# Kernel tuning notes

Hardware: AMD Instinct MI355X
Metric: run time of the kernel (lower is better)

The kernel has to match this reference:

```python
import jax, jax.numpy as jnp
import numpy as np

B, S, D = 2, 2048, 1024
H = 16
HD = D // H  # 64

def setup_inputs() -> dict:
    key = jax.random.key(0)
    ks = jax.random.split(key, 6)
    scale = 0.02
    x   = jax.random.normal(ks[0], (B, S, D), dtype=jnp.float32)
    Wq  = jax.random.normal(ks[1], (D, D), dtype=jnp.float32) * scale
    Wk  = jax.random.normal(ks[2], (D, D), dtype=jnp.float32) * scale
    Wv  = jax.random.normal(ks[3], (D, D), dtype=jnp.float32) * scale
    Wo  = jax.random.normal(ks[4], (D, D), dtype=jnp.float32) * scale
    bo  = jax.random.normal(ks[5], (D,), dtype=jnp.float32) * scale
    return {"x": x, "Wq": Wq, "Wk": Wk, "Wv": Wv, "Wo": Wo, "bo": bo}

def reference(x, Wq, Wk, Wv, Wo, bo):
    b, s, d = x.shape
    # QKV projections (no bias, qkv_bias=False); weights stored as [d_in, d_out]
    q = (x @ Wq).reshape(b, s, H, HD).transpose(0, 2, 1, 3)  # [b,h,s,hd]
    k = (x @ Wk).reshape(b, s, H, HD).transpose(0, 2, 1, 3)
    v = (x @ Wv).reshape(b, s, H, HD).transpose(0, 2, 1, 3)
    scores = jnp.einsum('bhqd,bhkd->bhqk', q, k)  # [b,h,s,s]
    causal = jnp.triu(jnp.ones((s, s), dtype=bool), k=1)
    scores = jnp.where(causal, -jnp.inf, scores)
    attn = jax.nn.softmax(scores / jnp.sqrt(jnp.float32(HD)), axis=-1)
    # dropout_rate = 0.0 -> identity
    ctx = jnp.einsum('bhqk,bhkd->bqhd', attn, v).reshape(b, s, d)
    return ctx @ Wo + bo
```

## Files before the change

### kernel.cpp

```cpp
#include <hip/hip_runtime.h>
#include <hip/hip_bf16.h>
#include <math.h>

#define B_ 2
#define S_ 2048
#define D_ 1024
#define H_ 16
#define HD_ 64
#define M_ (B_*S_)

typedef __attribute__((ext_vector_type(8))) short bf16x8;
typedef __attribute__((ext_vector_type(4))) float f32x4;
typedef __attribute__((ext_vector_type(16))) float f32x16;

#define MFMA16(a,b,c) __builtin_amdgcn_mfma_f32_16x16x32_bf16(a,b,c,0,0,0)
#define MFMA32(a,b,c) __builtin_amdgcn_mfma_f32_32x32x16_bf16(a,b,c,0,0,0)
#define INFF __builtin_inff()
#define LOG2E 1.44269504088896340736f
#define EXP2F(x) __builtin_amdgcn_exp2f(x)

static __device__ __forceinline__ unsigned short f2bf_bits(float f) {
    unsigned int u = __float_as_uint(f);
    unsigned int r = (u + 0x7fffu + ((u >> 16) & 1u)) >> 16;
    return (unsigned short)r;
}

static __device__ __forceinline__ unsigned cvt_pk_bf16(float a, float b) {
    unsigned r;
    asm("v_cvt_pk_bf16_f32 %0, %1, %2" : "=v"(r) : "v"(a), "v"(b));
    return r;
}

static __device__ __forceinline__ void gload16(const unsigned short* g, unsigned short* l) {
    __builtin_amdgcn_global_load_lds(
        (const __attribute__((address_space(1))) unsigned int*)(g),
        (__attribute__((address_space(3))) unsigned int*)(l),
        16, 0, 0);
}

#define BARR do { \
    __builtin_amdgcn_sched_barrier(0); \
    __builtin_amdgcn_s_barrier(); \
    __builtin_amdgcn_sched_barrier(0); \
} while (0)
#define LGK0 do { \
    asm volatile("s_waitcnt lgkmcnt(0)" ::: "memory"); \
    __builtin_amdgcn_sched_barrier(0); \
} while (0)
#define LGK8 do { \
    asm volatile("s_waitcnt lgkmcnt(8)" ::: "memory"); \
    __builtin_amdgcn_sched_barrier(0); \
} while (0)
#define VM6 do { \
    asm volatile("s_waitcnt vmcnt(6)" ::: "memory"); \
    __builtin_amdgcn_sched_barrier(0); \
} while (0)

__global__ __launch_bounds__(256) void convert_x_kernel(
    const float* __restrict__ x, unsigned short* __restrict__ o) {
    size_t i = (size_t)blockIdx.x * 256 + threadIdx.x;
    float4 v = reinterpret_cast<const float4*>(x)[i];
    ushort4 u;
    u.x = f2bf_bits(v.x); u.y = f2bf_bits(v.y);
    u.z = f2bf_bits(v.z); u.w = f2bf_bits(v.w);
    reinterpret_cast<ushort4*>(o)[i] = u;
}

__global__ __launch_bounds__(256) void convw_kernel(
    const float* __restrict__ W0, const float* __restrict__ W1,
    const float* __restrict__ W2, const float* __restrict__ W3,
    unsigned short* __restrict__ OT) {
    __shared__ float t[32][33];
    const float* W = (blockIdx.z == 0) ? W0 : (blockIdx.z == 1) ? W1
                    : (blockIdx.z == 2) ? W2 : W3;
    unsigned short* O = OT + (size_t)blockIdx.z * D_ * D_;
    int tx = threadIdx.x & 31, ty = threadIdx.x >> 5;
    int kb = blockIdx.y * 32, nb = blockIdx.x * 32;
#pragma unroll
    for (int i = 0; i < 4; i++)
        t[ty + 8*i][tx] = W[(size_t)(kb + ty + 8*i) * D_ + nb + tx];
    __syncthreads();
#pragma unroll
    for (int i = 0; i < 4; i++) {
        int n = nb + ty + 8*i, k = kb + tx;
        O[(size_t)n * D_ + k] = f2bf_bits(t[tx][ty + 8*i]);
    }
}

__global__ __launch_bounds__(512, 2) void gemm_qkv256(
    const unsigned short* __restrict__ A,
    const unsigned short* __restrict__ BT,
    unsigned short* __restrict__ outp)
{
    __shared__ union {
        struct { unsigned short A[2][2][8192]; unsigned short B[2][2][8192]; } s;
        unsigned short vt[256][136];
    } sm;
    const int tid = threadIdx.x, lane = tid & 63, wid = tid >> 6;
    const int lrow = lane & 15, lk8 = lane >> 4, orow = lk8 * 4;
    const int wmo = (wid >> 2) * 64;
    const int wno = (wid & 3) * 32;
    const int m0 = blockIdx.x * 256, n0 = blockIdx.y * 256;

    const int srow = lane >> 3, sgr = lane & 7;
    const unsigned sgo = (unsigned)(wid * 8 + srow) * 1024u
                       + (unsigned)((sgr ^ srow) << 3);
    const unsigned short* Ag = A  + (unsigned)m0 * 1024u + sgo;
    const unsigned short* Bg = BT + (unsigned)n0 * 1024u + sgo;
    const int ldsrb = wid * 512;

    const int sw0 = ((lk8 ^ (lrow & 7)) << 3);
    const int sw1 = (((4 | lk8) ^ (lrow & 7)) << 3);
    int ar[4], br[2];
#pragma unroll
    for (int f = 0; f < 4; f++) ar[f] = (wmo + f * 16 + lrow) * 64;
#pragma unroll
    for (int g = 0; g < 2; g++) br[g] = (wno + g * 16 + lrow) * 64;

    f32x4 acc[8][4] = {};
    bf16x8 af[4][2], bf0[2][2], bf1[2][2];

    auto stA = [&](int par, int mh, unsigned k) {
        unsigned short* d = &sm.s.A[par][mh][ldsrb];
        const unsigned short* g = Ag + (unsigned)mh * 131072u + k;
        gload16(g, d);
        gload16(g + 65536u, d + 4096);
    };
    auto stB = [&](int par, int nh, unsigned k) {
        unsigned short* d = &sm.s.B[par][nh][ldsrb];
        const unsigned short* g = Bg + (unsigned)nh * 131072u + k;
        gload16(g, d);
        gload16(g + 65536u, d + 4096);
    };
    auto lda = [&](int par, int mh) {
        const unsigned short* p = &sm.s.A[par][mh][0];
#pragma unroll
        for (int f = 0; f < 4; f++) {
            af[f][0] = *reinterpret_cast<const bf16x8*>(p + ar[f] + sw0);
            af[f][1] = *reinterpret_cast<const bf16x8*>(p + ar[f] + sw1);
        }
    };
    auto ldb0 = [&](int par, int nh) {
        const unsigned short* p = &sm.s.B[par][nh][0];
#pragma unroll
        for (int g = 0; g < 2; g++) {
            bf0[g][0] = *reinterpret_cast<const bf16x8*>(p + br[g] + sw0);
            bf0[g][1] = *reinterpret_cast<const bf16x8*>(p + br[g] + sw1);
        }
    };
    auto ldb1 = [&](int par, int nh) {
        const unsigned short* p = &sm.s.B[par][nh][0];
#pragma unroll
        for (int g = 0; g < 2; g++) {
            bf1[g][0] = *reinterpret_cast<const bf16x8*>(p + br[g] + sw0);
            bf1[g][1] = *reinterpret_cast<const bf16x8*>(p + br[g] + sw1);
        }
    };
    auto MMA0 = [&](int mh) {
        __builtin_amdgcn_s_setprio(1);
#pragma unroll
        for (int f = 0; f < 4; f++)
#pragma unroll
            for (int g = 0; g < 2; g++)
#pragma unroll
                for (int ks = 0; ks < 2; ks++)
                    acc[mh*4+f][g] = MFMA16(af[f][ks], bf0[g][ks], acc[mh*4+f][g]);
        __builtin_amdgcn_s_setprio(0);
    };
    auto MMA1 = [&](int mh) {
        __builtin_amdgcn_s_setprio(1);
#pragma unroll
        for (int f = 0; f < 4; f++)
#pragma unroll
            for (int g = 0; g < 2; g++)
#pragma unroll
                for (int ks = 0; ks < 2; ks++)
                    acc[mh*4+f][2+g] = MFMA16(af[f][ks], bf1[g][ks], acc[mh*4+f][2+g]);
        __builtin_amdgcn_s_setprio(0);
    };

    stA(0, 0, 0);  stB(0, 0, 0);  stB(0, 1, 0);  stA(0, 1, 0);
    stA(1, 0, 64); stB(1, 0, 64); stB(1, 1, 64);
    VM6; BARR;

#pragma unroll 1
    for (int i = 0; i < 8; i++) {
        const unsigned kA1 = (unsigned)(2*i + 1) * 64u;
        const unsigned k2  = (unsigned)((2*i + 2) & 15) * 64u;
        const unsigned k3  = (unsigned)((2*i + 3) & 15) * 64u;
        lda(0, 0); ldb0(0, 0); stA(1, 1, kA1);
        LGK8; BARR; LGK0; MMA0(0); BARR;
        ldb1(0, 1); stA(0, 0, k2);
        BARR; LGK0; MMA1(0); BARR;
        lda(0, 1); stB(0, 0, k2);
        BARR; LGK0; MMA1(1); BARR;
        stB(0, 1, k2);
        VM6; BARR; MMA0(1); BARR;
        lda(1, 0); ldb0(1, 0); stA(0, 1, k2);
        LGK8; BARR; LGK0; MMA0(0); BARR;
        ldb1(1, 1); stA(1, 0, k3);
        BARR; LGK0; MMA1(0); BARR;
        lda(1, 1); stB(1, 0, k3);
        BARR; LGK0; MMA1(1); BARR;
        stB(1, 1, k3);
        VM6; BARR; MMA0(1); BARR;
    }

    asm volatile("s_waitcnt vmcnt(0)" ::: "memory");
    __builtin_amdgcn_sched_barrier(0);
    __builtin_amdgcn_s_barrier();

    const int which = n0 >> 10;
    const int nl0 = n0 & 1023;
    const int bq = m0 >> 11;
    unsigned short* obase = outp + (size_t)which * 4194304;

    if (which < 2) {
        const float scale = (which == 0) ? (0.125f * LOG2E) : 1.0f;
#pragma unroll
        for (int fi = 0; fi < 8; fi++)
#pragma unroll
            for (int g = 0; g < 4; g++)
#pragma unroll
                for (int r = 0; r < 4; r++) {
                    int m = m0 + (fi >> 2) * 128 + wmo + (fi & 3) * 16 + orow + r;
                    int n = nl0 + (g >> 1) * 128 + wno + (g & 1) * 16 + lrow;
                    int s = m & 2047;
                    obase[(((size_t)(bq * 16 + (n >> 6)) * 2048 + s) << 6) + (n & 63)]
                        = f2bf_bits(acc[fi][g][r] * scale);
                }
    } else {
#pragma unroll
        for (int qm = 0; qm < 2; qm++) {
#pragma unroll
            for (int f = 0; f < 4; f++)
#pragma unroll
                for (int g = 0; g < 4; g++) {
                    const int ml = wmo + f * 16 + orow;
                    const int nc = (g >> 1) * 128 + wno + (g & 1) * 16 + lrow;
                    uint2 w;
                    w.x = cvt_pk_bf16(acc[qm*4+f][g][0], acc[qm*4+f][g][1]);
                    w.y = cvt_pk_bf16(acc[qm*4+f][g][2], acc[qm*4+f][g][3]);
                    *reinterpret_cast<uint2*>(&sm.vt[nc][ml]) = w;
                }
            __syncthreads();
            {
                const int row = tid >> 1, c0 = (tid & 1) * 64;
                unsigned short* dst = obase +
                    ((size_t)(bq * 1024) + nl0 + row) * 2048 +
                    (m0 & 2047) + qm * 128 + c0;
#pragma unroll
                for (int j = 0; j < 64; j += 8)
                    *reinterpret_cast<bf16x8*>(dst + j) =
                        *reinterpret_cast<const bf16x8*>(&sm.vt[row][c0 + j]);
            }
            __syncthreads();
        }
    }
}

template<int BN, int MODE>
__global__ __launch_bounds__(256) void gemm_gl(
    const unsigned short* __restrict__ A,
    const unsigned short* __restrict__ BT,
    void* __restrict__ outp,
    const float* __restrict__ bias)
{
    constexpr int K = 1024;
    constexpr int NF = (BN == 128) ? 4 : 2;
    __shared__ struct { unsigned short As[128][64]; unsigned short Bs[BN][64]; } sm;
    const int m0 = blockIdx.x * 128;
    const int n0 = blockIdx.y * BN;
    const int tid = threadIdx.x, lane = tid & 63, wid = tid >> 6;
    const int wm = (wid >> 1) * 64;
    const int wn = (wid & 1) * (BN / 2);
    const int lrow = lane & 15, lk8 = lane >> 4, orow = lk8 * 4;
    f32x4 acc[4][NF] = {};

    for (int k0 = 0; k0 < K; k0 += 64) {
#pragma unroll
        for (int i = 0; i < 4; i++) {
            const int rbase = wid * 32 + i * 8;
            const int rl = rbase + (lane >> 3);
            const int sc = ((lane & 7) ^ (rl & 7)) << 3;
            gload16(A + (size_t)(m0 + rl) * K + k0 + sc, &sm.As[rbase][0]);
        }
#pragma unroll
        for (int i = 0; i < BN / 32; i++) {
            const int rbase = wid * (BN / 4) + i * 8;
            const int rl = rbase + (lane >> 3);
            const int sc = ((lane & 7) ^ (rl & 7)) << 3;
            gload16(BT + (size_t)(n0 + rl) * K + k0 + sc, &sm.Bs[rbase][0]);
        }
        __syncthreads();
#pragma unroll
        for (int ks = 0; ks < 2; ks++) {
            bf16x8 af[4], bfr[NF];
#pragma unroll
            for (int f = 0; f < 4; f++) {
                const int row = wm + f * 16 + lrow;
                const int p = (ks * 4 + lk8) ^ (row & 7);
                af[f] = *reinterpret_cast<const bf16x8*>(&sm.As[row][p * 8]);
            }
#pragma unroll
            for (int f = 0; f < NF; f++) {
                const int row = wn + f * 16 + lrow;
                const int p = (ks * 4 + lk8) ^ (row & 7);
                bfr[f] = *reinterpret_cast<const bf16x8*>(&sm.Bs[row][p * 8]);
            }
            __builtin_amdgcn_s_setprio(1);
#pragma unroll
            for (int mf = 0; mf < 4; mf++)
#pragma unroll
                for (int nf = 0; nf < NF; nf++)
                    acc[mf][nf] = MFMA16(af[mf], bfr[nf], acc[mf][nf]);
            __builtin_amdgcn_s_setprio(0);
        }
        __syncthreads();
    }

    float* o = (float*)outp;
#pragma unroll
    for (int mf = 0; mf < 4; mf++)
#pragma unroll
        for (int nf = 0; nf < NF; nf++)
#pragma unroll
            for (int r = 0; r < 4; r++) {
                int m = m0 + wm + mf*16 + orow + r;
                int n = n0 + wn + nf*16 + lrow;
                o[(size_t)m * 1024 + n] = acc[mf][nf][r] + bias[n];
            }
}

__global__ __launch_bounds__(256, 2) void attn_kernel(
    const unsigned short* __restrict__ Q,
    const unsigned short* __restrict__ Kb,
    const unsigned short* __restrict__ VT,
    unsigned short* __restrict__ ctx)
{
    __shared__ unsigned short Ks[2][64][64];
    __shared__ unsigned short Vs[2][64][64];
    const int fid = blockIdx.x;
    const int xcd = fid & 7, t = fid >> 3;
    const int bh = xcd | ((t & 3) << 3);
    const int qt = 15 - (t >> 2);
    const int lane = threadIdx.x & 63, wid = threadIdx.x >> 6;
    const int l31 = lane & 31, hi = lane >> 5;
    const unsigned short* Qp = Q  + (size_t)bh * (S_ * 64);
    const unsigned short* Kp = Kb + (size_t)bh * (S_ * 64);
    const unsigned short* Vp = VT + (size_t)bh * (64 * S_);
    const int b = bh >> 4, h = bh & 15;
    const int q0w = qt * 128 + wid * 32;
    const int qg  = q0w + l31;
    const int nb  = 2 * qt + 2;

    auto stage = [&](int buf, int kv0) {
#pragma unroll
        for (int i = 0; i < 2; i++) {
            const int rbase = wid * 16 + 8 * i;
            const int rl = rbase + (lane >> 3);
            const int sc = (((lane & 7) ^ (rl & 7)) << 3);
            gload16(Kp + (size_t)(kv0 + rl) * 64 + sc, &Ks[buf][rbase][0]);
            gload16(Vp + (size_t)rl * S_ + kv0 + sc, &Vs[buf][rbase][0]);
        }
    };

    stage(0, 0);

    bf16x8 qf[4];
#pragma unroll
    for (int c = 0; c < 4; c++)
        qf[c] = *reinterpret_cast<const bf16x8*>(
            Qp + (size_t)qg * 64 + c * 16 + hi * 8);

    f32x16 oacc0 = {}, oacc1 = {};
    float lr = 0.f;
    const int r0 = l31, r1 = 32 + l31;
    const int g0 = r0 & 7, g1 = r1 & 7;

    __syncthreads();

#pragma unroll 1
    for (int kvb = 0; kvb < nb; kvb++) {
        const int cur = kvb & 1;
        if (kvb + 1 < nb) stage(cur ^ 1, (kvb + 1) * 64);

        f32x16 s0 = {}, s1 = {};
        __builtin_amdgcn_s_setprio(1);
#pragma unroll
        for (int c = 0; c < 4; c++) {
            const int gg = (c << 1) | hi;
            bf16x8 k0 = *reinterpret_cast<const bf16x8*>(&Ks[cur][r0][(gg ^ g0) << 3]);
            bf16x8 k1 = *reinterpret_cast<const bf16x8*>(&Ks[cur][r1][(gg ^ g1) << 3]);
            s0 = MFMA32(k0, qf[c], s0);
            s1 = MFMA32(k1, qf[c], s1);
        }
        __builtin_amdgcn_s_setprio(0);

        if (kvb * 64 + 63 > q0w) {
            const int kvb64 = kvb * 64 + 4 * hi;
#pragma unroll
            for (int reg = 0; reg < 16; reg++) {
                const int kv = kvb64 + (reg & 3) + 8 * (reg >> 2);
                if (kv > qg)      s0[reg] = -INFF;
                if (kv + 32 > qg) s1[reg] = -INFF;
            }
        }

        float t0 = 0.f, t1 = 0.f;
#pragma unroll
        for (int reg = 0; reg < 16; reg++) {
            s0[reg] = EXP2F(s0[reg]);
            s1[reg] = EXP2F(s1[reg]);
            t0 += s0[reg];
            t1 += s1[reg];
        }
        lr += t0 + t1;

        bf16x8 pf[4];
#pragma unroll
        for (int c = 0; c < 4; c++) {
            const int rb = (c & 1) * 8;
            unsigned x0, x1, y0, y1;
            if (c < 2) {
                x0 = cvt_pk_bf16(s0[rb+0], s0[rb+1]);
                x1 = cvt_pk_bf16(s0[rb+2], s0[rb+3]);
                y0 = cvt_pk_bf16(s0[rb+4], s0[rb+5]);
                y1 = cvt_pk_bf16(s0[rb+6], s0[rb+7]);
            } else {
                x0 = cvt_pk_bf16(s1[rb+0], s1[rb+1]);
                x1 = cvt_pk_bf16(s1[rb+2], s1[rb+3]);
                y0 = cvt_pk_bf16(s1[rb+4], s1[rb+5]);
                y1 = cvt_pk_bf16(s1[rb+6], s1[rb+7]);
            }
            asm("v_permlane32_swap_b32 %0, %1" : "+v"(x0), "+v"(y0));
            asm("v_permlane32_swap_b32 %0, %1" : "+v"(x1), "+v"(y1));
            union { unsigned u[4]; bf16x8 v; } pk;
            pk.u[0] = x0; pk.u[1] = x1; pk.u[2] = y0; pk.u[3] = y1;
            pf[c] = pk.v;
        }

        __builtin_amdgcn_s_setprio(1);
#pragma unroll
        for (int c = 0; c < 4; c++) {
            const int gg = (c << 1) | hi;
            bf16x8 v0 = *reinterpret_cast<const bf16x8*>(&Vs[cur][r0][(gg ^ g0) << 3]);
            bf16x8 v1 = *reinterpret_cast<const bf16x8*>(&Vs[cur][r1][(gg ^ g1) << 3]);
            oacc0 = MFMA32(v0, pf[c], oacc0);
            oacc1 = MFMA32(v1, pf[c], oacc1);
        }
        __builtin_amdgcn_s_setprio(0);
        __syncthreads();
    }

    lr += __shfl_xor(lr, 32);
    const float inv = 1.0f / lr;
    unsigned short* crow = ctx + ((size_t)(b * S_ + qg)) * D_ + h * 64;
#pragma unroll
    for (int a = 0; a < 4; a++)
#pragma unroll
        for (int p = 0; p < 2; p++) {
            const int reg = 4 * a + 2 * p;
            const int col = 8 * a + 4 * hi + 2 * p;
            unsigned w0 = cvt_pk_bf16(oacc0[reg] * inv, oacc0[reg + 1] * inv);
            unsigned w1 = cvt_pk_bf16(oacc1[reg] * inv, oacc1[reg + 1] * inv);
            *reinterpret_cast<unsigned*>(crow + col)      = w0;
            *reinterpret_cast<unsigned*>(crow + 32 + col) = w1;
        }
}

extern "C" void kernel_launch(void* const* d_in, const int* in_sizes, int n_in,
                              void* d_out, int out_size, void* d_ws, size_t ws_size,
                              hipStream_t stream) {
    const float* x  = (const float*)d_in[0];
    const float* Wq = (const float*)d_in[1];
    const float* Wk = (const float*)d_in[2];
    const float* Wv = (const float*)d_in[3];
    const float* Wo = (const float*)d_in[4];
    const float* bo = (const float*)d_in[5];
    float* out = (float*)d_out;

    char* ws = (char*)d_ws;
    unsigned short* xb  = (unsigned short*)(ws);
    unsigned short* WT  = (unsigned short*)(ws + 8388608);
    unsigned short* QKV = (unsigned short*)(ws + 16777216);
    unsigned short* ctx = (unsigned short*)(ws + 41943040);

    unsigned short* Qb  = QKV;
    unsigned short* Kb  = QKV + 4194304;
    unsigned short* VTb = QKV + 8388608;

    convert_x_kernel<<<dim3(4096), dim3(256), 0, stream>>>(x, xb);
    convw_kernel<<<dim3(32, 32, 4), dim3(256), 0, stream>>>(Wq, Wk, Wv, Wo, WT);

    gemm_qkv256<<<dim3(16, 12), dim3(512), 0, stream>>>(xb, WT, QKV);

    attn_kernel<<<dim3(512), dim3(256), 0, stream>>>(Qb, Kb, VTb, ctx);

    gemm_gl<128, 1><<<dim3(32, 8), dim3(256), 0, stream>>>(
        ctx, WT + 3145728, (void*)out, bo);
}
```

Before: 111.8 us.

## Split attention into single-wave blocks loading K/V directly from global

The attention kernel becomes one 64-thread wave per 32-query tile with 2048 blocks. The LDS double-buffered staging and the block barriers are removed, and each lane now loads its K and V fragments straight from global memory. The causal mask is applied only on the last KV block, and the output GEMM switches to a 64-wide tile with twice as many blocks. The aim is finer causal load balance and no cross-wave synchronisation. The cost is that K/V are no longer shared through LDS, so each wave issues redundant global/L2 reads with little overlap of load latency.

Result: slower. 136.3 us (+22.0%).

```diff
diff --git a/kernel.cpp b/kernel.cpp
--- a/kernel.cpp
+++ b/kernel.cpp
@@ -332,40 +332,25 @@
             }
 }
 
-__global__ __launch_bounds__(256, 2) void attn_kernel(
+__global__ __launch_bounds__(64, 3) void attn_kernel(
     const unsigned short* __restrict__ Q,
     const unsigned short* __restrict__ Kb,
     const unsigned short* __restrict__ VT,
     unsigned short* __restrict__ ctx)
 {
-    __shared__ unsigned short Ks[2][64][64];
-    __shared__ unsigned short Vs[2][64][64];
     const int fid = blockIdx.x;
     const int xcd = fid & 7, t = fid >> 3;
     const int bh = xcd | ((t & 3) << 3);
-    const int qt = 15 - (t >> 2);
-    const int lane = threadIdx.x & 63, wid = threadIdx.x >> 6;
+    const int qt = 63 - (t >> 2);
+    const int lane = threadIdx.x;
     const int l31 = lane & 31, hi = lane >> 5;
     const unsigned short* Qp = Q  + (size_t)bh * (S_ * 64);
     const unsigned short* Kp = Kb + (size_t)bh * (S_ * 64);
     const unsigned short* Vp = VT + (size_t)bh * (64 * S_);
     const int b = bh >> 4, h = bh & 15;
-    const int q0w = qt * 128 + wid * 32;
-    const int qg  = q0w + l31;
-    const int nb  = 2 * qt + 2;
-
-    auto stage = [&](int buf, int kv0) {
-#pragma unroll
-        for (int i = 0; i < 2; i++) {
-            const int rbase = wid * 16 + 8 * i;
-            const int rl = rbase + (lane >> 3);
-            const int sc = (((lane & 7) ^ (rl & 7)) << 3);
-            gload16(Kp + (size_t)(kv0 + rl) * 64 + sc, &Ks[buf][rbase][0]);
-            gload16(Vp + (size_t)rl * S_ + kv0 + sc, &Vs[buf][rbase][0]);
-        }
-    };
-
-    stage(0, 0);
+    const int qg = qt * 32 + l31;
+    const int nb = qt / 2 + 1;
+    const int r0 = l31, r1 = 32 + l31;
 
     bf16x8 qf[4];
 #pragma unroll
@@ -375,30 +360,41 @@
 
     f32x16 oacc0 = {}, oacc1 = {};
     float lr = 0.f;
-    const int r0 = l31, r1 = 32 + l31;
-    const int g0 = r0 & 7, g1 = r1 & 7;
-
-    __syncthreads();
 
 #pragma unroll 1
     for (int kvb = 0; kvb < nb; kvb++) {
-        const int cur = kvb & 1;
-        if (kvb + 1 < nb) stage(cur ^ 1, (kvb + 1) * 64);
-
+        const unsigned kv0 = (unsigned)kvb * 64u;
+
+        bf16x8 kf0[4], kf1[4];
+#pragma unroll
+        for (int c = 0; c < 4; c++) {
+            const unsigned gg = ((unsigned)c << 1) | (unsigned)hi;
+            kf0[c] = *reinterpret_cast<const bf16x8*>(
+                Kp + (size_t)(kv0 + r0) * 64 + gg * 8);
+            kf1[c] = *reinterpret_cast<const bf16x8*>(
+                Kp + (size_t)(kv0 + r1) * 64 + gg * 8);
+        }
         f32x16 s0 = {}, s1 = {};
         __builtin_amdgcn_s_setprio(1);
 #pragma unroll
         for (int c = 0; c < 4; c++) {
-            const int gg = (c << 1) | hi;
-            bf16x8 k0 = *reinterpret_cast<const bf16x8*>(&Ks[cur][r0][(gg ^ g0) << 3]);
-            bf16x8 k1 = *reinterpret_cast<const bf16x8*>(&Ks[cur][r1][(gg ^ g1) << 3]);
-            s0 = MFMA32(k0, qf[c], s0);
-            s1 = MFMA32(k1, qf[c], s1);
+            s0 = MFMA32(kf0[c], qf[c], s0);
+            s1 = MFMA32(kf1[c], qf[c], s1);
         }
         __builtin_amdgcn_s_setprio(0);
 
-        if (kvb * 64 + 63 > q0w) {
-            const int kvb64 = kvb * 64 + 4 * hi;
+        bf16x8 vf0[4], vf1[4];
+#pragma unroll
+        for (int c = 0; c < 4; c++) {
+            const unsigned gg = ((unsigned)c << 1) | (unsigned)hi;
+            vf0[c] = *reinterpret_cast<const bf16x8*>(
+                Vp + (size_t)r0 * S_ + kv0 + gg * 8);
+            vf1[c] = *reinterpret_cast<const bf16x8*>(
+                Vp + (size_t)r1 * S_ + kv0 + gg * 8);
+        }
+
+        if (kvb == nb - 1) {
+            const int kvb64 = (int)kv0 + 4 * hi;
 #pragma unroll
             for (int reg = 0; reg < 16; reg++) {
                 const int kv = kvb64 + (reg & 3) + 8 * (reg >> 2);
@@ -443,14 +439,10 @@
         __builtin_amdgcn_s_setprio(1);
 #pragma unroll
         for (int c = 0; c < 4; c++) {
-            const int gg = (c << 1) | hi;
-            bf16x8 v0 = *reinterpret_cast<const bf16x8*>(&Vs[cur][r0][(gg ^ g0) << 3]);
-            bf16x8 v1 = *reinterpret_cast<const bf16x8*>(&Vs[cur][r1][(gg ^ g1) << 3]);
-            oacc0 = MFMA32(v0, pf[c], oacc0);
-            oacc1 = MFMA32(v1, pf[c], oacc1);
+            oacc0 = MFMA32(vf0[c], pf[c], oacc0);
+            oacc1 = MFMA32(vf1[c], pf[c], oacc1);
         }
         __builtin_amdgcn_s_setprio(0);
-        __syncthreads();
     }
 
     lr += __shfl_xor(lr, 32);
@@ -495,8 +487,8 @@
 
     gemm_qkv256<<<dim3(16, 12), dim3(512), 0, stream>>>(xb, WT, QKV);
 
-    attn_kernel<<<dim3(512), dim3(256), 0, stream>>>(Qb, Kb, VTb, ctx);
-
-    gemm_gl<128, 1><<<dim3(32, 8), dim3(256), 0, stream>>>(
+    attn_kernel<<<dim3(2048), dim3(64), 0, stream>>>(Qb, Kb, VTb, ctx);
+
+    gemm_gl<64, 1><<<dim3(32, 16), dim3(256), 0, stream>>>(
         ctx, WT + 3145728, (void*)out, bo);
 }
```

## Split KV across wave pairs and pair causal q-tiles per block for balance

Applied to the files above, without the earlier changes.

The attention kernel now processes 64-row query tiles, and each block handles a complementary pair of tiles (jp and 31-jp) so that every block does the same amount of causal work. Within a block, waves are paired: each pair covers 32 query rows and splits every 64-wide KV block into two 32-column halves. The partial outputs and row sums from the two halves are merged through a shared-memory buffer unioned with the K/V staging area. This targets load imbalance across blocks and halves the per-wave score registers. In exchange it adds an extra reduction through LDS, extra barriers, and a second pipeline warm-up per block.

Result: slower. 115.0 us (+2.8%).

```diff
diff --git a/kernel.cpp b/kernel.cpp
--- a/kernel.cpp
+++ b/kernel.cpp
@@ -338,21 +338,25 @@
     const unsigned short* __restrict__ VT,
     unsigned short* __restrict__ ctx)
 {
-    __shared__ unsigned short Ks[2][64][64];
-    __shared__ unsigned short Vs[2][64][64];
+    __shared__ union {
+        struct { unsigned short Ks[2][64][64]; unsigned short Vs[2][64][64]; } t;
+        float mg[2][64][34];
+    } sm;
     const int fid = blockIdx.x;
-    const int xcd = fid & 7, t = fid >> 3;
-    const int bh = xcd | ((t & 3) << 3);
-    const int qt = 15 - (t >> 2);
+    const int xcd = fid & 7, tt = fid >> 3;
+    const int bh = xcd | ((tt & 3) << 3);
+    const int jp = tt >> 2;
     const int lane = threadIdx.x & 63, wid = threadIdx.x >> 6;
+    const int qw = wid >> 1, kh = wid & 1;
     const int l31 = lane & 31, hi = lane >> 5;
     const unsigned short* Qp = Q  + (size_t)bh * (S_ * 64);
     const unsigned short* Kp = Kb + (size_t)bh * (S_ * 64);
     const unsigned short* Vp = VT + (size_t)bh * (64 * S_);
     const int b = bh >> 4, h = bh & 15;
-    const int q0w = qt * 128 + wid * 32;
-    const int qg  = q0w + l31;
-    const int nb  = 2 * qt + 2;
+
+    const int rK = kh * 32 + l31, gK = rK & 7;
+    const int rV0 = l31, rV1 = 32 + l31;
+    const int gV0 = rV0 & 7, gV1 = rV1 & 7;
 
     auto stage = [&](int buf, int kv0) {
 #pragma unroll
@@ -360,113 +364,129 @@
             const int rbase = wid * 16 + 8 * i;
             const int rl = rbase + (lane >> 3);
             const int sc = (((lane & 7) ^ (rl & 7)) << 3);
-            gload16(Kp + (size_t)(kv0 + rl) * 64 + sc, &Ks[buf][rbase][0]);
-            gload16(Vp + (size_t)rl * S_ + kv0 + sc, &Vs[buf][rbase][0]);
-        }
-    };
-
-    stage(0, 0);
-
-    bf16x8 qf[4];
-#pragma unroll
-    for (int c = 0; c < 4; c++)
-        qf[c] = *reinterpret_cast<const bf16x8*>(
-            Qp + (size_t)qg * 64 + c * 16 + hi * 8);
-
-    f32x16 oacc0 = {}, oacc1 = {};
-    float lr = 0.f;
-    const int r0 = l31, r1 = 32 + l31;
-    const int g0 = r0 & 7, g1 = r1 & 7;
-
-    __syncthreads();
+            gload16(Kp + (size_t)(kv0 + rl) * 64 + sc, &sm.t.Ks[buf][rbase][0]);
+            gload16(Vp + (size_t)rl * S_ + kv0 + sc, &sm.t.Vs[buf][rbase][0]);
+        }
+    };
 
 #pragma unroll 1
-    for (int kvb = 0; kvb < nb; kvb++) {
-        const int cur = kvb & 1;
-        if (kvb + 1 < nb) stage(cur ^ 1, (kvb + 1) * 64);
-
-        f32x16 s0 = {}, s1 = {};
-        __builtin_amdgcn_s_setprio(1);
-#pragma unroll
-        for (int c = 0; c < 4; c++) {
-            const int gg = (c << 1) | hi;
-            bf16x8 k0 = *reinterpret_cast<const bf16x8*>(&Ks[cur][r0][(gg ^ g0) << 3]);
-            bf16x8 k1 = *reinterpret_cast<const bf16x8*>(&Ks[cur][r1][(gg ^ g1) << 3]);
-            s0 = MFMA32(k0, qf[c], s0);
-            s1 = MFMA32(k1, qf[c], s1);
-        }
-        __builtin_amdgcn_s_setprio(0);
-
-        if (kvb * 64 + 63 > q0w) {
-            const int kvb64 = kvb * 64 + 4 * hi;
+    for (int half = 0; half < 2; half++) {
+        const int qt = half ? (31 - jp) : jp;
+        const int nb = qt + 1;
+        const int q0w = qt * 64 + qw * 32;
+        const int qg = q0w + l31;
+
+        stage(0, 0);
+
+        bf16x8 qf[4];
+#pragma unroll
+        for (int c = 0; c < 4; c++)
+            qf[c] = *reinterpret_cast<const bf16x8*>(
+                Qp + (size_t)qg * 64 + c * 16 + hi * 8);
+
+        f32x16 oacc0 = {}, oacc1 = {};
+        float lr = 0.f;
+
+        __syncthreads();
+
+#pragma unroll 1
+        for (int kvb = 0; kvb < nb; kvb++) {
+            const int cur = kvb & 1;
+            if (kvb + 1 < nb) stage(cur ^ 1, (kvb + 1) * 64);
+
+            f32x16 s = {};
+            __builtin_amdgcn_s_setprio(1);
+#pragma unroll
+            for (int c = 0; c < 4; c++) {
+                const int gg = (c << 1) | hi;
+                bf16x8 kf = *reinterpret_cast<const bf16x8*>(
+                    &sm.t.Ks[cur][rK][(gg ^ gK) << 3]);
+                s = MFMA32(kf, qf[c], s);
+            }
+            __builtin_amdgcn_s_setprio(0);
+
+            if (kvb == qt) {
+                const int kb0 = kvb * 64 + kh * 32 + 4 * hi;
+#pragma unroll
+                for (int reg = 0; reg < 16; reg++) {
+                    const int kv = kb0 + (reg & 3) + 8 * (reg >> 2);
+                    if (kv > qg) s[reg] = -INFF;
+                }
+            }
+
+            float tsum = 0.f;
 #pragma unroll
             for (int reg = 0; reg < 16; reg++) {
-                const int kv = kvb64 + (reg & 3) + 8 * (reg >> 2);
-                if (kv > qg)      s0[reg] = -INFF;
-                if (kv + 32 > qg) s1[reg] = -INFF;
-            }
-        }
-
-        float t0 = 0.f, t1 = 0.f;
-#pragma unroll
-        for (int reg = 0; reg < 16; reg++) {
-            s0[reg] = EXP2F(s0[reg]);
-            s1[reg] = EXP2F(s1[reg]);
-            t0 += s0[reg];
-            t1 += s1[reg];
-        }
-        lr += t0 + t1;
-
-        bf16x8 pf[4];
-#pragma unroll
-        for (int c = 0; c < 4; c++) {
-            const int rb = (c & 1) * 8;
-            unsigned x0, x1, y0, y1;
-            if (c < 2) {
-                x0 = cvt_pk_bf16(s0[rb+0], s0[rb+1]);
-                x1 = cvt_pk_bf16(s0[rb+2], s0[rb+3]);
-                y0 = cvt_pk_bf16(s0[rb+4], s0[rb+5]);
-                y1 = cvt_pk_bf16(s0[rb+6], s0[rb+7]);
-            } else {
-                x0 = cvt_pk_bf16(s1[rb+0], s1[rb+1]);
-                x1 = cvt_pk_bf16(s1[rb+2], s1[rb+3]);
-                y0 = cvt_pk_bf16(s1[rb+4], s1[rb+5]);
-                y1 = cvt_pk_bf16(s1[rb+6], s1[rb+7]);
-            }
-            asm("v_permlane32_swap_b32 %0, %1" : "+v"(x0), "+v"(y0));
-            asm("v_permlane32_swap_b32 %0, %1" : "+v"(x1), "+v"(y1));
-            union { unsigned u[4]; bf16x8 v; } pk;
-            pk.u[0] = x0; pk.u[1] = x1; pk.u[2] = y0; pk.u[3] = y1;
-            pf[c] = pk.v;
-        }
-
-        __builtin_amdgcn_s_setprio(1);
-#pragma unroll
-        for (int c = 0; c < 4; c++) {
-            const int gg = (c << 1) | hi;
-            bf16x8 v0 = *reinterpret_cast<const bf16x8*>(&Vs[cur][r0][(gg ^ g0) << 3]);
-            bf16x8 v1 = *reinterpret_cast<const bf16x8*>(&Vs[cur][r1][(gg ^ g1) << 3]);
-            oacc0 = MFMA32(v0, pf[c], oacc0);
-            oacc1 = MFMA32(v1, pf[c], oacc1);
-        }
-        __builtin_amdgcn_s_setprio(0);
+                s[reg] = EXP2F(s[reg]);
+                tsum += s[reg];
+            }
+            lr += tsum;
+
+            bf16x8 pf[2];
+#pragma unroll
+            for (int c = 0; c < 2; c++) {
+                const int rb = c * 8;
+                unsigned x0 = cvt_pk_bf16(s[rb+0], s[rb+1]);
+                unsigned x1 = cvt_pk_bf16(s[rb+2], s[rb+3]);
+                unsigned y0 = cvt_pk_bf16(s[rb+4], s[rb+5]);
+                unsigned y1 = cvt_pk_bf16(s[rb+6], s[rb+7]);
+                asm("v_permlane32_swap_b32 %0, %1" : "+v"(x0), "+v"(y0));
+                asm("v_permlane32_swap_b32 %0, %1" : "+v"(x1), "+v"(y1));
+                union { unsigned u[4]; bf16x8 v; } pk;
+                pk.u[0] = x0; pk.u[1] = x1; pk.u[2] = y0; pk.u[3] = y1;
+                pf[c] = pk.v;
+            }
+
+            __builtin_amdgcn_s_setprio(1);
+#pragma unroll
+            for (int c = 0; c < 2; c++) {
+                const int gg = 4 * kh + 2 * c + hi;
+                bf16x8 v0 = *reinterpret_cast<const bf16x8*>(
+                    &sm.t.Vs[cur][rV0][(gg ^ gV0) << 3]);
+                bf16x8 v1 = *reinterpret_cast<const bf16x8*>(
+                    &sm.t.Vs[cur][rV1][(gg ^ gV1) << 3]);
+                oacc0 = MFMA32(v0, pf[c], oacc0);
+                oacc1 = MFMA32(v1, pf[c], oacc1);
+            }
+            __builtin_amdgcn_s_setprio(0);
+            __syncthreads();
+        }
+
+        lr += __shfl_xor(lr, 32);
+        if (kh == 1) {
+            float* m = &sm.mg[qw][0][0];
+#pragma unroll
+            for (int r = 0; r < 16; r++) {
+                m[lane * 34 + r]      = oacc0[r];
+                m[lane * 34 + 16 + r] = oacc1[r];
+            }
+            m[lane * 34 + 32] = lr;
+        }
+        __syncthreads();
+        if (kh == 0) {
+            const float* m = &sm.mg[qw][0][0];
+#pragma unroll
+            for (int r = 0; r < 16; r++) {
+                oacc0[r] += m[lane * 34 + r];
+                oacc1[r] += m[lane * 34 + 16 + r];
+            }
+            lr += m[lane * 34 + 32];
+            const float inv = 1.0f / lr;
+            unsigned short* crow = ctx + ((size_t)(b * S_ + qg)) * D_ + h * 64;
+#pragma unroll
+            for (int a = 0; a < 4; a++)
+#pragma unroll
+                for (int p = 0; p < 2; p++) {
+                    const int reg = 4 * a + 2 * p;
+                    const int col = 8 * a + 4 * hi + 2 * p;
+                    unsigned w0 = cvt_pk_bf16(oacc0[reg] * inv, oacc0[reg+1] * inv);
+                    unsigned w1 = cvt_pk_bf16(oacc1[reg] * inv, oacc1[reg+1] * inv);
+                    *reinterpret_cast<unsigned*>(crow + col)      = w0;
+                    *reinterpret_cast<unsigned*>(crow + 32 + col) = w1;
+                }
+        }
         __syncthreads();
     }
-
-    lr += __shfl_xor(lr, 32);
-    const float inv = 1.0f / lr;
-    unsigned short* crow = ctx + ((size_t)(b * S_ + qg)) * D_ + h * 64;
-#pragma unroll
-    for (int a = 0; a < 4; a++)
-#pragma unroll
-        for (int p = 0; p < 2; p++) {
-            const int reg = 4 * a + 2 * p;
-            const int col = 8 * a + 4 * hi + 2 * p;
-            unsigned w0 = cvt_pk_bf16(oacc0[reg] * inv, oacc0[reg + 1] * inv);
-            unsigned w1 = cvt_pk_bf16(oacc1[reg] * inv, oacc1[reg + 1] * inv);
-            *reinterpret_cast<unsigned*>(crow + col)      = w0;
-            *reinterpret_cast<unsigned*>(crow + 32 + col) = w1;
-        }
 }
 
 extern "C" void kernel_launch(void* const* d_in, const int* in_sizes, int n_in,
```
